# Optimization experiments

Measured on AMD Instinct MI355X. Metric: run time of the kernel, lower is better.

The kernel has to match this reference:

```python
import jax, jax.numpy as jnp
import numpy as np

N = 50000        # nodes
E = 800000       # edges (avg degree 16)
OBS = 128        # observation_dim
HID = 64         # hidden_dim (per head)
H1 = 4           # heads in conv1
ACT = 32         # action_dim
NEG_SLOPE = 0.2  # GATv2 default negative_slope


def setup_inputs() -> dict:
    key = jax.random.key(0)
    ks = jax.random.split(key, 10)
    s = 0.05
    x = jax.random.normal(ks[0], (N, OBS), jnp.float32)
    edge_index = jax.random.randint(ks[1], (2, E), 0, N, dtype=jnp.int32)
    # conv1: GATv2Conv(OBS -> HID, heads=4, concat=True)
    W1l = jax.random.normal(ks[2], (OBS, H1 * HID), jnp.float32) * s  # lin_l (source)
    W1r = jax.random.normal(ks[3], (OBS, H1 * HID), jnp.float32) * s  # lin_r (target)
    att1 = jax.random.normal(ks[4], (H1, HID), jnp.float32) * s
    b1 = jnp.zeros((H1 * HID,), jnp.float32)
    # conv2: GATv2Conv(H1*HID -> ACT, heads=1, concat=False)
    W2l = jax.random.normal(ks[5], (H1 * HID, ACT), jnp.float32) * s
    W2r = jax.random.normal(ks[6], (H1 * HID, ACT), jnp.float32) * s
    att2 = jax.random.normal(ks[7], (1, ACT), jnp.float32) * s
    b2 = jnp.zeros((ACT,), jnp.float32)
    return {"x": x, "edge_index": edge_index, "W1l": W1l, "W1r": W1r,
            "att1": att1, "b1": b1, "W2l": W2l, "W2r": W2r,
            "att2": att2, "b2": b2}


def gatv2_layer(x, Wl, Wr, att, bias, src, dst, heads, out_ch, concat):
    """PyG GATv2Conv (add_self_loops=False, share_weights=False)."""
    n = x.shape[0]
    xl = (x @ Wl).reshape(n, heads, out_ch)  # source transform
    xr = (x @ Wr).reshape(n, heads, out_ch)  # target transform
    e = xl[src] + xr[dst]                    # [E, H, C] gathered messages
    g = jnp.where(e > 0, e, NEG_SLOPE * e)   # LeakyReLU
    logits = jnp.einsum('ehc,hc->eh', g, att)  # [E, H]
    # segment softmax over incoming edges of each destination node
    m = jax.ops.segment_max(logits, dst, num_segments=n)      # [N, H]
    ex = jnp.exp(logits - m[dst])
    denom = jax.ops.segment_sum(ex, dst, num_segments=n)      # [N, H]
    alpha = ex / denom[dst]                                   # [E, H]
    out = jax.ops.segment_sum(xl[src] * alpha[:, :, None], dst, num_segments=n)
    out = out.reshape(n, heads * out_ch) if concat else out.mean(axis=1)
    return out + bias


def reference(x, edge_index, W1l, W1r, att1, b1, W2l, W2r, att2, b2):
    src, dst = edge_index[0], edge_index[1]
    h = jax.nn.relu(gatv2_layer(x, W1l, W1r, att1, b1, src, dst, H1, HID, True))
    out = gatv2_layer(h, W2l, W2r, att2, b2, src, dst, 1, ACT, False)
    return out
```

## Files before the change

kernel.cpp:

```cpp
#include <hip/hip_runtime.h>
#include <hip/hip_bf16.h>
#include <math.h>


#define OBS 128
#define HID 64
#define H1 4
#define C1 256
#define ACT 32
#define PAD 128
#define NEG_SLOPE 0.2f
#define LOG2E 1.4426950408889634f
#define SB 512
#define CAP 8192
#define AGGB 2048

typedef __attribute__((ext_vector_type(2))) _Float16 h2;
typedef __attribute__((ext_vector_type(8))) _Float16 half8;
typedef __attribute__((ext_vector_type(4))) float f32x4;

__device__ inline h2 bc_h2(unsigned u) { return __builtin_bit_cast(h2, u); }
__device__ inline unsigned bc_u(h2 v) { return __builtin_bit_cast(unsigned, v); }
__device__ inline h2 lrelu2(h2 e) {
  const h2 k = {(_Float16)NEG_SLOPE, (_Float16)NEG_SLOPE};
  return __builtin_elementwise_max(e, e * k);
}

__global__ void prep0(const float* __restrict__ W1l, const float* __restrict__ W1r,
                      const float* __restrict__ W2l, const float* __restrict__ W2r,
                      _Float16* __restrict__ W1t, _Float16* __restrict__ W2t,
                      unsigned* __restrict__ bucketCursor) {
  int i = blockIdx.x * 256 + threadIdx.x;
  if (i < 256) bucketCursor[i] = 0;
  if (i < 512 * 128) {
    int n = i >> 7, k = i & 127;
    float v = (n < C1) ? W1l[k * C1 + n] : W1r[k * C1 + (n - C1)];
    W1t[i] = (_Float16)v;
  }
  int j = i - 512 * 128;
  if (j >= 0 && j < 64 * 256) {
    int n = j >> 8, c = j & 255;
    float v = (n < ACT) ? W2l[c * ACT + n] : W2r[c * ACT + (n - ACT)];
    W2t[j] = (_Float16)v;
  }
}

__global__ __launch_bounds__(256) void scat2_k(const int* __restrict__ src,
                                               const int* __restrict__ dst,
                                               unsigned* __restrict__ bucketCursor,
                                               unsigned* __restrict__ sorted,
                                               int E, int epb) {
  __shared__ unsigned cnt[256];
  __shared__ unsigned lbase[256];
  __shared__ unsigned lrank[256];
  int t = threadIdx.x;
  cnt[t] = 0;
  lrank[t] = 0;
  __syncthreads();
  int beg = blockIdx.x * epb;
  int end = beg + epb;
  if (end > E) end = E;
  for (int e = beg + t; e < end; e += 256)
    atomicAdd(&cnt[dst[e] >> 8], 1u);
  __syncthreads();
  unsigned c = cnt[t];
  lbase[t] = c ? atomicAdd(&bucketCursor[t], c) : 0u;
  __syncthreads();
  for (int e = beg + t; e < end; e += 256) {
    int d = dst[e];
    int sv = src[e];
    int b = d >> 8;
    unsigned r = atomicAdd(&lrank[b], 1u);
    sorted[(size_t)b * CAP + lbase[b] + r] =
        ((unsigned)(d & 255) << 16) | (unsigned)sv;
  }
}

__global__ __launch_bounds__(256) void bcsr_k(const unsigned* __restrict__ sorted,
                                              const unsigned* __restrict__ bucketCursor,
                                              unsigned short* __restrict__ esrc_p,
                                              int* __restrict__ cursor, int N) {
  __shared__ unsigned cnt2[256];
  int b = blockIdx.x;
  int t = threadIdx.x;
  cnt2[t] = 0;
  __syncthreads();
  unsigned total = bucketCursor[b];
  const unsigned* sp = sorted + (size_t)b * CAP;
  for (unsigned e = t; e < total; e += 256) {
    unsigned u = sp[e];
    unsigned dl = u >> 16;
    unsigned slot = atomicAdd(&cnt2[dl], 1u);
    if (slot < PAD)
      esrc_p[((size_t)((b << 8) + (int)dl) << 7) + slot] =
          (unsigned short)(u & 0xFFFFu);
  }
  __syncthreads();
  int node = (b << 8) + t;
  if (node < N) cursor[node] = (int)cnt2[t];
}

__global__ __launch_bounds__(256) void gemm1(
    const float* __restrict__ xf,
    const _Float16* __restrict__ W1t,
    _Float16* __restrict__ XLh,
    _Float16* __restrict__ XRh,
    int M) {
  const int LDK = 136;
  __shared__ _Float16 As[128 * 136];
  __shared__ _Float16 Bs[128 * 136];

  const int tid = threadIdx.x;
  const int lane = tid & 63;
  const int wid = tid >> 6;
  const int wm = (wid & 1) * 64, wn = (wid >> 1) * 64;
  const int rowBase = blockIdx.x * 128;
  const int l15 = lane & 15, lq = lane >> 4;

#pragma unroll
  for (int cc = 0; cc < 8; ++cc) {
    int q = cc * 256 + tid;
    int r = q >> 4;
    int kc = (q & 15) * 8;
    int grow = rowBase + r;
    float4 f0 = make_float4(0.f, 0.f, 0.f, 0.f), f1 = f0;
    if (grow < M) {
      f0 = *(const float4*)(xf + (size_t)grow * 128 + kc);
      f1 = *(const float4*)(xf + (size_t)grow * 128 + kc + 4);
    }
    h2 p0 = {(_Float16)f0.x, (_Float16)f0.y};
    h2 p1 = {(_Float16)f0.z, (_Float16)f0.w};
    h2 p2 = {(_Float16)f1.x, (_Float16)f1.y};
    h2 p3 = {(_Float16)f1.z, (_Float16)f1.w};
    *(int4*)(As + r * LDK + kc) = make_int4(bc_u(p0), bc_u(p1), bc_u(p2), bc_u(p3));
  }
#pragma unroll
  for (int cc = 0; cc < 8; ++cc) {
    int q = cc * 256 + tid;
    int r = q >> 4;
    int kc = (q & 15) * 8;
    *(int4*)(Bs + r * LDK + kc) = *(const int4*)(W1t + (size_t)r * 128 + kc);
  }
  __syncthreads();

  for (int cb = 0; cb < 4; ++cb) {
    f32x4 acc[4][4];
#pragma unroll
    for (int i = 0; i < 4; ++i)
#pragma unroll
      for (int j = 0; j < 4; ++j) acc[i][j] = (f32x4){0.f, 0.f, 0.f, 0.f};

#pragma unroll
    for (int ks = 0; ks < 4; ++ks) {
      half8 af[4], bf[4];
#pragma unroll
      for (int t = 0; t < 4; ++t) {
        af[t] = *(const half8*)(As + (wm + t * 16 + l15) * LDK + ks * 32 + lq * 8);
        bf[t] = *(const half8*)(Bs + (wn + t * 16 + l15) * LDK + ks * 32 + lq * 8);
      }
#pragma unroll
      for (int mt = 0; mt < 4; ++mt)
#pragma unroll
        for (int nt = 0; nt < 4; ++nt)
          acc[mt][nt] = __builtin_amdgcn_mfma_f32_16x16x32_f16(
              af[mt], bf[nt], acc[mt][nt], 0, 0, 0);
    }

    _Float16* outp = (cb < 2) ? XLh : XRh;
    int colBase = (cb & 1) * 128;
#pragma unroll
    for (int mt = 0; mt < 4; ++mt) {
#pragma unroll
      for (int r = 0; r < 4; ++r) {
        int row = rowBase + wm + mt * 16 + lq * 4 + r;
        if (row >= M) continue;
#pragma unroll
        for (int nt = 0; nt < 4; ++nt) {
          int col = colBase + wn + nt * 16 + l15;
          outp[(size_t)row * C1 + col] = (_Float16)acc[mt][nt][r];
        }
      }
    }

    if (cb < 3) {
      __syncthreads();
#pragma unroll
      for (int cc = 0; cc < 8; ++cc) {
        int q = cc * 256 + tid;
        int r = q >> 4;
        int kc = (q & 15) * 8;
        *(int4*)(Bs + r * LDK + kc) =
            *(const int4*)(W1t + (size_t)((cb + 1) * 128 + r) * 128 + kc);
      }
      __syncthreads();
    }
  }
}

__global__ __launch_bounds__(256) void gemm_mfma2(
    const _Float16* __restrict__ Hh,
    const _Float16* __restrict__ W2t,
    _Float16* __restrict__ H2h,
    int M) {
  const int LDK = 136;
  __shared__ _Float16 As[128 * 136];
  __shared__ _Float16 Bs[64 * 136];
  const int tid = threadIdx.x;
  const int lane = tid & 63;
  const int wid = tid >> 6;
  const int wm = (wid & 1) * 64, wn = (wid >> 1) * 32;
  const int rowBase = blockIdx.x * 128;

  f32x4 acc[4][2];
#pragma unroll
  for (int i = 0; i < 4; ++i)
#pragma unroll
    for (int j = 0; j < 2; ++j) acc[i][j] = (f32x4){0.f, 0.f, 0.f, 0.f};

  const int l15 = lane & 15, lq = lane >> 4;

  for (int kb = 0; kb < 256; kb += 128) {
#pragma unroll
    for (int cc = 0; cc < 8; ++cc) {
      int q = cc * 256 + tid;
      int r = q >> 4;
      int kc = (q & 15) * 8;
      int grow = rowBase + r;
      int4 av = make_int4(0, 0, 0, 0);
      if (grow < M) av = *(const int4*)(Hh + (size_t)grow * 256 + kb + kc);
      *(int4*)(As + r * LDK + kc) = av;
    }
#pragma unroll
    for (int cc = 0; cc < 4; ++cc) {
      int q = cc * 256 + tid;
      int r = q >> 4;
      int kc = (q & 15) * 8;
      *(int4*)(Bs + r * LDK + kc) = *(const int4*)(W2t + (size_t)r * 256 + kb + kc);
    }
    __syncthreads();

#pragma unroll
    for (int ks = 0; ks < 4; ++ks) {
      half8 af[4], bf[2];
#pragma unroll
      for (int t = 0; t < 4; ++t)
        af[t] = *(const half8*)(As + (wm + t * 16 + l15) * LDK + ks * 32 + lq * 8);
#pragma unroll
      for (int t = 0; t < 2; ++t)
        bf[t] = *(const half8*)(Bs + (wn + t * 16 + l15) * LDK + ks * 32 + lq * 8);
#pragma unroll
      for (int mt = 0; mt < 4; ++mt)
#pragma unroll
        for (int nt = 0; nt < 2; ++nt)
          acc[mt][nt] = __builtin_amdgcn_mfma_f32_16x16x32_f16(
              af[mt], bf[nt], acc[mt][nt], 0, 0, 0);
    }
    __syncthreads();
  }

#pragma unroll
  for (int mt = 0; mt < 4; ++mt) {
#pragma unroll
    for (int r = 0; r < 4; ++r) {
      int row = rowBase + wm + mt * 16 + lq * 4 + r;
      if (row >= M) continue;
#pragma unroll
      for (int nt = 0; nt < 2; ++nt) {
        int col = wn + nt * 16 + l15;
        H2h[(size_t)row * 64 + col] = (_Float16)acc[mt][nt][r];
      }
    }
  }
}

__global__ __launch_bounds__(256) void agg1(const _Float16* __restrict__ XLh,
                                            const _Float16* XRh,
                                            const float* __restrict__ att1,
                                            const float* __restrict__ b1,
                                            const int* __restrict__ degp,
                                            const unsigned short* __restrict__ esrc_p,
                                            _Float16* Hh, int n_nodes) {
  int wave = threadIdx.x >> 6;
  int lane = threadIdx.x & 63;
  int wgid = blockIdx.x * 4 + wave;
  int W = gridDim.x * 4;
  int sl = lane & 31;
  int half = lane >> 5;
  int c8 = sl * 8;

  const char* XLb = (const char*)XLh + c8 * 2;
  const float* ap = att1 + (c8 >> 6) * HID + (c8 & 63);
  float4 a0 = *(const float4*)ap;
  float4 a1 = *(const float4*)(ap + 4);
  h2 av[4] = {{(_Float16)(a0.x * LOG2E), (_Float16)(a0.y * LOG2E)},
              {(_Float16)(a0.z * LOG2E), (_Float16)(a0.w * LOG2E)},
              {(_Float16)(a1.x * LOG2E), (_Float16)(a1.y * LOG2E)},
              {(_Float16)(a1.z * LOG2E), (_Float16)(a1.w * LOG2E)}};
  float4 b0 = *(const float4*)(b1 + c8);
  float4 b3 = *(const float4*)(b1 + c8 + 4);

  for (int n = wgid; n < n_nodes; n += W) {
    int4 xru = *(const int4*)((const char*)XRh + ((size_t)n << 9) + c8 * 2);
    h2 xr[4] = {bc_h2(xru.x), bc_h2(xru.y), bc_h2(xru.z), bc_h2(xru.w)};

    int d = min(degp[n], PAD);
    const unsigned short* ep = esrc_p + ((size_t)n << 7);
    float l = 0.f;
    h2 acc[4];
#pragma unroll
    for (int k = 0; k < 4; ++k) acc[k] = (h2){(_Float16)0.f, (_Float16)0.f};

    int base = 0;
    for (; base + 16 <= d; base += 16) {
      int4 u[8];
#pragma unroll
      for (int t = 0; t < 8; ++t) {
        int s = ep[base + 2 * t + half];
        u[t] = *(const int4*)(XLb + ((size_t)s << 9));
      }
      float c[8];
#pragma unroll
      for (int t = 0; t < 8; ++t) {
        h2 xa = bc_h2(u[t].x), xb = bc_h2(u[t].y), xc = bc_h2(u[t].z), xd = bc_h2(u[t].w);
        float cc = __builtin_amdgcn_fdot2(lrelu2(xa + xr[0]), av[0], 0.f, false);
        cc = __builtin_amdgcn_fdot2(lrelu2(xb + xr[1]), av[1], cc, false);
        cc = __builtin_amdgcn_fdot2(lrelu2(xc + xr[2]), av[2], cc, false);
        cc = __builtin_amdgcn_fdot2(lrelu2(xd + xr[3]), av[3], cc, false);
        c[t] = cc;
      }
#pragma unroll
      for (int t = 0; t < 8; ++t) {
        c[t] += __shfl_xor(c[t], 1);
        c[t] += __shfl_xor(c[t], 2);
        c[t] += __shfl_xor(c[t], 4);
      }
#pragma unroll
      for (int t = 0; t < 8; ++t) {
        float p = __builtin_amdgcn_exp2f(c[t]);
        l += p;
        _Float16 ph = (_Float16)p;
        h2 w = {ph, ph};
        acc[0] = acc[0] + w * bc_h2(u[t].x);
        acc[1] = acc[1] + w * bc_h2(u[t].y);
        acc[2] = acc[2] + w * bc_h2(u[t].z);
        acc[3] = acc[3] + w * bc_h2(u[t].w);
      }
    }
    for (; base + 4 <= d; base += 4) {
      int s0 = ep[base + half];
      int s1 = ep[base + 2 + half];
      int4 u0 = *(const int4*)(XLb + ((size_t)s0 << 9));
      int4 u1 = *(const int4*)(XLb + ((size_t)s1 << 9));
      h2 x0[4] = {bc_h2(u0.x), bc_h2(u0.y), bc_h2(u0.z), bc_h2(u0.w)};
      h2 x1[4] = {bc_h2(u1.x), bc_h2(u1.y), bc_h2(u1.z), bc_h2(u1.w)};
      float c0 = 0.f, c1 = 0.f;
#pragma unroll
      for (int k = 0; k < 4; ++k) {
        c0 = __builtin_amdgcn_fdot2(lrelu2(x0[k] + xr[k]), av[k], c0, false);
        c1 = __builtin_amdgcn_fdot2(lrelu2(x1[k] + xr[k]), av[k], c1, false);
      }
      c0 += __shfl_xor(c0, 1); c1 += __shfl_xor(c1, 1);
      c0 += __shfl_xor(c0, 2); c1 += __shfl_xor(c1, 2);
      c0 += __shfl_xor(c0, 4); c1 += __shfl_xor(c1, 4);
      float p0 = __builtin_amdgcn_exp2f(c0);
      float p1 = __builtin_amdgcn_exp2f(c1);
      l += p0 + p1;
      _Float16 q0 = (_Float16)p0, q1 = (_Float16)p1;
      h2 w0 = {q0, q0}, w1 = {q1, q1};
#pragma unroll
      for (int k = 0; k < 4; ++k) acc[k] = acc[k] + w0 * x0[k] + w1 * x1[k];
    }
    if (base < d) {
      int e0 = base + half, e1 = base + 2 + half;
      bool v0 = e0 < d, v1 = e1 < d;
      int s0 = ep[v0 ? e0 : 0];
      int s1 = ep[v1 ? e1 : 0];
      int4 u0 = *(const int4*)(XLb + ((size_t)s0 << 9));
      int4 u1 = *(const int4*)(XLb + ((size_t)s1 << 9));
      h2 x0[4] = {bc_h2(u0.x), bc_h2(u0.y), bc_h2(u0.z), bc_h2(u0.w)};
      h2 x1[4] = {bc_h2(u1.x), bc_h2(u1.y), bc_h2(u1.z), bc_h2(u1.w)};
      float c0 = 0.f, c1 = 0.f;
#pragma unroll
      for (int k = 0; k < 4; ++k) {
        c0 = __builtin_amdgcn_fdot2(lrelu2(x0[k] + xr[k]), av[k], c0, false);
        c1 = __builtin_amdgcn_fdot2(lrelu2(x1[k] + xr[k]), av[k], c1, false);
      }
      c0 += __shfl_xor(c0, 1); c1 += __shfl_xor(c1, 1);
      c0 += __shfl_xor(c0, 2); c1 += __shfl_xor(c1, 2);
      c0 += __shfl_xor(c0, 4); c1 += __shfl_xor(c1, 4);
      float p0 = v0 ? __builtin_amdgcn_exp2f(c0) : 0.f;
      float p1 = v1 ? __builtin_amdgcn_exp2f(c1) : 0.f;
      l += p0 + p1;
      _Float16 q0 = (_Float16)p0, q1 = (_Float16)p1;
      h2 w0 = {q0, q0}, w1 = {q1, q1};
#pragma unroll
      for (int k = 0; k < 4; ++k) acc[k] = acc[k] + w0 * x0[k] + w1 * x1[k];
    }

    l += __shfl_xor(l, 32);
#pragma unroll
    for (int k = 0; k < 4; ++k) {
      unsigned o = __shfl_xor((int)bc_u(acc[k]), 32);
      acc[k] = acc[k] + bc_h2(o);
    }

    float inv = (d > 0) ? 1.f / l : 0.f;
    if (half == 0) {
      float o0 = fmaxf((float)acc[0][0] * inv + b0.x, 0.f);
      float o1 = fmaxf((float)acc[0][1] * inv + b0.y, 0.f);
      float o2 = fmaxf((float)acc[1][0] * inv + b0.z, 0.f);
      float o3 = fmaxf((float)acc[1][1] * inv + b0.w, 0.f);
      float o4 = fmaxf((float)acc[2][0] * inv + b3.x, 0.f);
      float o5 = fmaxf((float)acc[2][1] * inv + b3.y, 0.f);
      float o6 = fmaxf((float)acc[3][0] * inv + b3.z, 0.f);
      float o7 = fmaxf((float)acc[3][1] * inv + b3.w, 0.f);
      h2 q0 = {(_Float16)o0, (_Float16)o1};
      h2 q1 = {(_Float16)o2, (_Float16)o3};
      h2 q2 = {(_Float16)o4, (_Float16)o5};
      h2 q3 = {(_Float16)o6, (_Float16)o7};
      *(int4*)((char*)Hh + ((size_t)n << 9) + c8 * 2) =
          make_int4(bc_u(q0), bc_u(q1), bc_u(q2), bc_u(q3));
    }
  }
}

__global__ __launch_bounds__(256) void agg2(const _Float16* __restrict__ H2h,
                                            const float* __restrict__ att2,
                                            const float* __restrict__ b2,
                                            const int* __restrict__ degp,
                                            const unsigned short* __restrict__ esrc_p,
                                            float* __restrict__ out, int n_nodes) {
  int wave = threadIdx.x >> 6;
  int lane = threadIdx.x & 63;
  int wgid = blockIdx.x * 4 + wave;
  int W = gridDim.x * 4;
  int g = lane >> 3;
  int j = lane & 7;
  int c4 = j * 4;

  const char* Hb = (const char*)H2h + c4 * 2;
  float4 af = *(const float4*)(att2 + c4);
  h2 a0 = {(_Float16)(af.x * LOG2E), (_Float16)(af.y * LOG2E)};
  h2 a1 = {(_Float16)(af.z * LOG2E), (_Float16)(af.w * LOG2E)};
  float4 bb = *(const float4*)(b2 + c4);

  for (int n = wgid; n < n_nodes; n += W) {
    uint2 hru = *(const uint2*)((const char*)H2h + ((size_t)n << 7) + 64 + c4 * 2);
    h2 hr0 = bc_h2(hru.x), hr1 = bc_h2(hru.y);

    int d = min(degp[n], PAD);
    const unsigned short* ep = esrc_p + ((size_t)n << 7);
    float l = 0.f;
    h2 acc0 = {(_Float16)0.f, (_Float16)0.f}, acc1 = acc0;

    int base = 0;
    for (; base + 16 <= d; base += 16) {
      int s0 = ep[base + g];
      int s1 = ep[base + 8 + g];
      uint2 u0 = *(const uint2*)(Hb + ((size_t)s0 << 7));
      uint2 u1 = *(const uint2*)(Hb + ((size_t)s1 << 7));
      h2 h00 = bc_h2(u0.x), h01 = bc_h2(u0.y);
      h2 h10 = bc_h2(u1.x), h11 = bc_h2(u1.y);
      float c0 = __builtin_amdgcn_fdot2(lrelu2(h00 + hr0), a0,
                 __builtin_amdgcn_fdot2(lrelu2(h01 + hr1), a1, 0.f, false), false);
      float c1 = __builtin_amdgcn_fdot2(lrelu2(h10 + hr0), a0,
                 __builtin_amdgcn_fdot2(lrelu2(h11 + hr1), a1, 0.f, false), false);
      c0 += __shfl_xor(c0, 1); c1 += __shfl_xor(c1, 1);
      c0 += __shfl_xor(c0, 2); c1 += __shfl_xor(c1, 2);
      c0 += __shfl_xor(c0, 4); c1 += __shfl_xor(c1, 4);
      float p0 = __builtin_amdgcn_exp2f(c0);
      float p1 = __builtin_amdgcn_exp2f(c1);
      l += p0 + p1;
      _Float16 q0 = (_Float16)p0, q1 = (_Float16)p1;
      h2 w0 = {q0, q0}, w1 = {q1, q1};
      acc0 = acc0 + w0 * h00 + w1 * h10;
      acc1 = acc1 + w0 * h01 + w1 * h11;
    }
    for (; base + 8 <= d; base += 8) {
      int s = ep[base + g];
      uint2 u = *(const uint2*)(Hb + ((size_t)s << 7));
      h2 h0 = bc_h2(u.x), h1 = bc_h2(u.y);
      float c = __builtin_amdgcn_fdot2(lrelu2(h0 + hr0), a0,
                __builtin_amdgcn_fdot2(lrelu2(h1 + hr1), a1, 0.f, false), false);
      c += __shfl_xor(c, 1);
      c += __shfl_xor(c, 2);
      c += __shfl_xor(c, 4);
      float p = __builtin_amdgcn_exp2f(c);
      l += p;
      _Float16 ph = (_Float16)p;
      h2 p2 = {ph, ph};
      acc0 = acc0 + p2 * h0;
      acc1 = acc1 + p2 * h1;
    }
    if (base < d) {
      int e = base + g;
      bool v = e < d;
      int s = ep[v ? e : 0];
      uint2 u = *(const uint2*)(Hb + ((size_t)s << 7));
      h2 h0 = bc_h2(u.x), h1 = bc_h2(u.y);
      float c = __builtin_amdgcn_fdot2(lrelu2(h0 + hr0), a0,
                __builtin_amdgcn_fdot2(lrelu2(h1 + hr1), a1, 0.f, false), false);
      c += __shfl_xor(c, 1);
      c += __shfl_xor(c, 2);
      c += __shfl_xor(c, 4);
      float p = v ? __builtin_amdgcn_exp2f(c) : 0.f;
      l += p;
      _Float16 ph = (_Float16)p;
      h2 p2 = {ph, ph};
      acc0 = acc0 + p2 * h0;
      acc1 = acc1 + p2 * h1;
    }

#pragma unroll
    for (int o = 8; o < 64; o <<= 1) {
      l += __shfl_xor(l, o);
      acc0 = acc0 + bc_h2((unsigned)__shfl_xor((int)bc_u(acc0), o));
      acc1 = acc1 + bc_h2((unsigned)__shfl_xor((int)bc_u(acc1), o));
    }

    float inv = (d > 0) ? 1.f / l : 0.f;
    if (g == 0) {
      float4 o;
      o.x = (float)acc0[0] * inv + bb.x;
      o.y = (float)acc0[1] * inv + bb.y;
      o.z = (float)acc1[0] * inv + bb.z;
      o.w = (float)acc1[1] * inv + bb.w;
      *(float4*)(out + (size_t)n * ACT + c4) = o;
    }
  }
}

extern "C" void kernel_launch(void* const* d_in, const int* in_sizes, int n_in,
                              void* d_out, int out_size, void* d_ws, size_t ws_size,
                              hipStream_t stream) {
  (void)n_in; (void)out_size; (void)ws_size;
  const float* x    = (const float*)d_in[0];
  const int*   ei   = (const int*)d_in[1];
  const float* W1l  = (const float*)d_in[2];
  const float* W1r  = (const float*)d_in[3];
  const float* att1 = (const float*)d_in[4];
  const float* b1   = (const float*)d_in[5];
  const float* W2l  = (const float*)d_in[6];
  const float* W2r  = (const float*)d_in[7];
  const float* att2 = (const float*)d_in[8];
  const float* b2   = (const float*)d_in[9];
  float* out = (float*)d_out;

  const int N = in_sizes[0] / OBS;
  const int E = in_sizes[1] / 2;
  const int* src = ei;
  const int* dst = ei + E;

  _Float16* XLh = (_Float16*)d_ws;
  _Float16* XRh = XLh + (size_t)N * C1;
  _Float16* W1t = XRh + (size_t)N * C1;
  _Float16* W2t = W1t + 512 * 128;
  int* cursor   = (int*)(W2t + 64 * 256);
  unsigned short* esrc_p = (unsigned short*)(cursor + N);
  _Float16* Hh  = XRh;
  _Float16* H2h = XLh;

  unsigned* sortedW = (unsigned*)d_ws;
  unsigned* bcur    = sortedW + 256 * CAP;

  dim3 b256(256);
  int gemmBlocks = (N + 127) / 128;
  int prepBlocks = (512 * 128 + 64 * 256 + 255) / 256;
  int NB = (N + 255) >> 8;
  int epb = (E + SB - 1) / SB;
  int aggBlocks = AGGB;
  if (aggBlocks * 4 > N) aggBlocks = (N + 3) / 4;

  prep0<<<prepBlocks, b256, 0, stream>>>(W1l, W1r, W2l, W2r, W1t, W2t, bcur);
  scat2_k<<<SB, b256, 0, stream>>>(src, dst, bcur, sortedW, E, epb);
  bcsr_k<<<NB, b256, 0, stream>>>(sortedW, bcur, esrc_p, cursor, N);
  gemm1<<<gemmBlocks, b256, 0, stream>>>(x, W1t, XLh, XRh, N);
  agg1<<<aggBlocks, b256, 0, stream>>>(XLh, XRh, att1, b1, cursor, esrc_p, Hh, N);
  gemm_mfma2<<<gemmBlocks, b256, 0, stream>>>(Hh, W2t, H2h, N);
  agg2<<<aggBlocks, b256, 0, stream>>>(H2h, att2, b2, cursor, esrc_p, out, N);
}
```

Before: 224.5 us.

## Split agg1 into one wave per node-head with eight edges gathered in parallel

The layer-1 aggregation kernel moves from a persistent grid-stride loop, where one wave covers all 256 channels of a node and two edges at a time, to a launch where each wave handles one (node, head) pair. Eight lanes cover the 64 channels of the head and eight edge groups run in parallel, followed by a cross-group shuffle reduction. Blocks are ordered head-major, so concurrently running waves gather only a 128-byte slice of XL per edge, which should improve cache locality and parallelism. The cost is a much larger grid (about 50k blocks), per-head reloads of degree and edge lists, and fewer gathers in flight per lane than the old 16-edge unrolled loop.

After: 249.8 us. +11.3%, slower.

```diff
diff --git a/kernel.cpp b/kernel.cpp
--- a/kernel.cpp
+++ b/kernel.cpp
@@ -279,148 +279,127 @@
                                             const float* __restrict__ b1,
                                             const int* __restrict__ degp,
                                             const unsigned short* __restrict__ esrc_p,
-                                            _Float16* Hh, int n_nodes) {
+                                            _Float16* Hh, int n_nodes, int nb) {
   int wave = threadIdx.x >> 6;
   int lane = threadIdx.x & 63;
-  int wgid = blockIdx.x * 4 + wave;
-  int W = gridDim.x * 4;
-  int sl = lane & 31;
-  int half = lane >> 5;
-  int c8 = sl * 8;
-
-  const char* XLb = (const char*)XLh + c8 * 2;
-  const float* ap = att1 + (c8 >> 6) * HID + (c8 & 63);
+  int head = blockIdx.x / nb;
+  int n = (blockIdx.x - head * nb) * 4 + wave;
+  if (n >= n_nodes) return;
+  int g = lane >> 3;
+  int j = lane & 7;
+  int cb = head * 128 + j * 16;
+
+  const char* XLb = (const char*)XLh + cb;
+  int4 xru = *(const int4*)((const char*)XRh + ((size_t)n << 9) + cb);
+  h2 xr[4] = {bc_h2(xru.x), bc_h2(xru.y), bc_h2(xru.z), bc_h2(xru.w)};
+  const float* ap = att1 + head * HID + j * 8;
   float4 a0 = *(const float4*)ap;
   float4 a1 = *(const float4*)(ap + 4);
   h2 av[4] = {{(_Float16)(a0.x * LOG2E), (_Float16)(a0.y * LOG2E)},
               {(_Float16)(a0.z * LOG2E), (_Float16)(a0.w * LOG2E)},
               {(_Float16)(a1.x * LOG2E), (_Float16)(a1.y * LOG2E)},
               {(_Float16)(a1.z * LOG2E), (_Float16)(a1.w * LOG2E)}};
-  float4 b0 = *(const float4*)(b1 + c8);
-  float4 b3 = *(const float4*)(b1 + c8 + 4);
-
-  for (int n = wgid; n < n_nodes; n += W) {
-    int4 xru = *(const int4*)((const char*)XRh + ((size_t)n << 9) + c8 * 2);
-    h2 xr[4] = {bc_h2(xru.x), bc_h2(xru.y), bc_h2(xru.z), bc_h2(xru.w)};
-
-    int d = min(degp[n], PAD);
-    const unsigned short* ep = esrc_p + ((size_t)n << 7);
-    float l = 0.f;
-    h2 acc[4];
-#pragma unroll
-    for (int k = 0; k < 4; ++k) acc[k] = (h2){(_Float16)0.f, (_Float16)0.f};
-
-    int base = 0;
-    for (; base + 16 <= d; base += 16) {
-      int4 u[8];
-#pragma unroll
-      for (int t = 0; t < 8; ++t) {
-        int s = ep[base + 2 * t + half];
-        u[t] = *(const int4*)(XLb + ((size_t)s << 9));
-      }
-      float c[8];
-#pragma unroll
-      for (int t = 0; t < 8; ++t) {
-        h2 xa = bc_h2(u[t].x), xb = bc_h2(u[t].y), xc = bc_h2(u[t].z), xd = bc_h2(u[t].w);
-        float cc = __builtin_amdgcn_fdot2(lrelu2(xa + xr[0]), av[0], 0.f, false);
-        cc = __builtin_amdgcn_fdot2(lrelu2(xb + xr[1]), av[1], cc, false);
-        cc = __builtin_amdgcn_fdot2(lrelu2(xc + xr[2]), av[2], cc, false);
-        cc = __builtin_amdgcn_fdot2(lrelu2(xd + xr[3]), av[3], cc, false);
-        c[t] = cc;
-      }
-#pragma unroll
-      for (int t = 0; t < 8; ++t) {
-        c[t] += __shfl_xor(c[t], 1);
-        c[t] += __shfl_xor(c[t], 2);
-        c[t] += __shfl_xor(c[t], 4);
-      }
-#pragma unroll
-      for (int t = 0; t < 8; ++t) {
-        float p = __builtin_amdgcn_exp2f(c[t]);
-        l += p;
-        _Float16 ph = (_Float16)p;
-        h2 w = {ph, ph};
-        acc[0] = acc[0] + w * bc_h2(u[t].x);
-        acc[1] = acc[1] + w * bc_h2(u[t].y);
-        acc[2] = acc[2] + w * bc_h2(u[t].z);
-        acc[3] = acc[3] + w * bc_h2(u[t].w);
-      }
-    }
-    for (; base + 4 <= d; base += 4) {
-      int s0 = ep[base + half];
-      int s1 = ep[base + 2 + half];
-      int4 u0 = *(const int4*)(XLb + ((size_t)s0 << 9));
-      int4 u1 = *(const int4*)(XLb + ((size_t)s1 << 9));
-      h2 x0[4] = {bc_h2(u0.x), bc_h2(u0.y), bc_h2(u0.z), bc_h2(u0.w)};
-      h2 x1[4] = {bc_h2(u1.x), bc_h2(u1.y), bc_h2(u1.z), bc_h2(u1.w)};
-      float c0 = 0.f, c1 = 0.f;
-#pragma unroll
-      for (int k = 0; k < 4; ++k) {
-        c0 = __builtin_amdgcn_fdot2(lrelu2(x0[k] + xr[k]), av[k], c0, false);
-        c1 = __builtin_amdgcn_fdot2(lrelu2(x1[k] + xr[k]), av[k], c1, false);
-      }
-      c0 += __shfl_xor(c0, 1); c1 += __shfl_xor(c1, 1);
-      c0 += __shfl_xor(c0, 2); c1 += __shfl_xor(c1, 2);
-      c0 += __shfl_xor(c0, 4); c1 += __shfl_xor(c1, 4);
-      float p0 = __builtin_amdgcn_exp2f(c0);
-      float p1 = __builtin_amdgcn_exp2f(c1);
-      l += p0 + p1;
-      _Float16 q0 = (_Float16)p0, q1 = (_Float16)p1;
-      h2 w0 = {q0, q0}, w1 = {q1, q1};
-#pragma unroll
-      for (int k = 0; k < 4; ++k) acc[k] = acc[k] + w0 * x0[k] + w1 * x1[k];
-    }
-    if (base < d) {
-      int e0 = base + half, e1 = base + 2 + half;
-      bool v0 = e0 < d, v1 = e1 < d;
-      int s0 = ep[v0 ? e0 : 0];
-      int s1 = ep[v1 ? e1 : 0];
-      int4 u0 = *(const int4*)(XLb + ((size_t)s0 << 9));
-      int4 u1 = *(const int4*)(XLb + ((size_t)s1 << 9));
-      h2 x0[4] = {bc_h2(u0.x), bc_h2(u0.y), bc_h2(u0.z), bc_h2(u0.w)};
-      h2 x1[4] = {bc_h2(u1.x), bc_h2(u1.y), bc_h2(u1.z), bc_h2(u1.w)};
-      float c0 = 0.f, c1 = 0.f;
-#pragma unroll
-      for (int k = 0; k < 4; ++k) {
-        c0 = __builtin_amdgcn_fdot2(lrelu2(x0[k] + xr[k]), av[k], c0, false);
-        c1 = __builtin_amdgcn_fdot2(lrelu2(x1[k] + xr[k]), av[k], c1, false);
-      }
-      c0 += __shfl_xor(c0, 1); c1 += __shfl_xor(c1, 1);
-      c0 += __shfl_xor(c0, 2); c1 += __shfl_xor(c1, 2);
-      c0 += __shfl_xor(c0, 4); c1 += __shfl_xor(c1, 4);
-      float p0 = v0 ? __builtin_amdgcn_exp2f(c0) : 0.f;
-      float p1 = v1 ? __builtin_amdgcn_exp2f(c1) : 0.f;
-      l += p0 + p1;
-      _Float16 q0 = (_Float16)p0, q1 = (_Float16)p1;
-      h2 w0 = {q0, q0}, w1 = {q1, q1};
-#pragma unroll
-      for (int k = 0; k < 4; ++k) acc[k] = acc[k] + w0 * x0[k] + w1 * x1[k];
-    }
-
-    l += __shfl_xor(l, 32);
+
+  int d = min(degp[n], PAD);
+  const unsigned short* ep = esrc_p + ((size_t)n << 7);
+  float l = 0.f;
+  h2 acc[4];
+#pragma unroll
+  for (int k = 0; k < 4; ++k) acc[k] = (h2){(_Float16)0.f, (_Float16)0.f};
+
+  int base = 0;
+  for (; base + 16 <= d; base += 16) {
+    int s0 = ep[base + g];
+    int s1 = ep[base + 8 + g];
+    int4 u0 = *(const int4*)(XLb + ((size_t)s0 << 9));
+    int4 u1 = *(const int4*)(XLb + ((size_t)s1 << 9));
+    h2 x0[4] = {bc_h2(u0.x), bc_h2(u0.y), bc_h2(u0.z), bc_h2(u0.w)};
+    h2 x1[4] = {bc_h2(u1.x), bc_h2(u1.y), bc_h2(u1.z), bc_h2(u1.w)};
+    float c0 = 0.f, c1 = 0.f;
 #pragma unroll
     for (int k = 0; k < 4; ++k) {
-      unsigned o = __shfl_xor((int)bc_u(acc[k]), 32);
-      acc[k] = acc[k] + bc_h2(o);
-    }
-
-    float inv = (d > 0) ? 1.f / l : 0.f;
-    if (half == 0) {
-      float o0 = fmaxf((float)acc[0][0] * inv + b0.x, 0.f);
-      float o1 = fmaxf((float)acc[0][1] * inv + b0.y, 0.f);
-      float o2 = fmaxf((float)acc[1][0] * inv + b0.z, 0.f);
-      float o3 = fmaxf((float)acc[1][1] * inv + b0.w, 0.f);
-      float o4 = fmaxf((float)acc[2][0] * inv + b3.x, 0.f);
-      float o5 = fmaxf((float)acc[2][1] * inv + b3.y, 0.f);
-      float o6 = fmaxf((float)acc[3][0] * inv + b3.z, 0.f);
-      float o7 = fmaxf((float)acc[3][1] * inv + b3.w, 0.f);
-      h2 q0 = {(_Float16)o0, (_Float16)o1};
-      h2 q1 = {(_Float16)o2, (_Float16)o3};
-      h2 q2 = {(_Float16)o4, (_Float16)o5};
-      h2 q3 = {(_Float16)o6, (_Float16)o7};
-      *(int4*)((char*)Hh + ((size_t)n << 9) + c8 * 2) =
-          make_int4(bc_u(q0), bc_u(q1), bc_u(q2), bc_u(q3));
-    }
+      c0 = __builtin_amdgcn_fdot2(lrelu2(x0[k] + xr[k]), av[k], c0, false);
+      c1 = __builtin_amdgcn_fdot2(lrelu2(x1[k] + xr[k]), av[k], c1, false);
+    }
+    c0 += __shfl_xor(c0, 1); c1 += __shfl_xor(c1, 1);
+    c0 += __shfl_xor(c0, 2); c1 += __shfl_xor(c1, 2);
+    c0 += __shfl_xor(c0, 4); c1 += __shfl_xor(c1, 4);
+    float p0 = __builtin_amdgcn_exp2f(c0);
+    float p1 = __builtin_amdgcn_exp2f(c1);
+    l += p0 + p1;
+    _Float16 q0 = (_Float16)p0, q1 = (_Float16)p1;
+    h2 w0 = {q0, q0}, w1 = {q1, q1};
+#pragma unroll
+    for (int k = 0; k < 4; ++k) acc[k] = acc[k] + w0 * x0[k] + w1 * x1[k];
+  }
+  for (; base + 8 <= d; base += 8) {
+    int s = ep[base + g];
+    int4 u = *(const int4*)(XLb + ((size_t)s << 9));
+    h2 x0[4] = {bc_h2(u.x), bc_h2(u.y), bc_h2(u.z), bc_h2(u.w)};
+    float c0 = 0.f;
+#pragma unroll
+    for (int k = 0; k < 4; ++k)
+      c0 = __builtin_amdgcn_fdot2(lrelu2(x0[k] + xr[k]), av[k], c0, false);
+    c0 += __shfl_xor(c0, 1);
+    c0 += __shfl_xor(c0, 2);
+    c0 += __shfl_xor(c0, 4);
+    float p0 = __builtin_amdgcn_exp2f(c0);
+    l += p0;
+    _Float16 q0 = (_Float16)p0;
+    h2 w0 = {q0, q0};
+#pragma unroll
+    for (int k = 0; k < 4; ++k) acc[k] = acc[k] + w0 * x0[k];
+  }
+  if (base < d) {
+    int e = base + g;
+    bool v = e < d;
+    int s = ep[v ? e : 0];
+    int4 u = *(const int4*)(XLb + ((size_t)s << 9));
+    h2 x0[4] = {bc_h2(u.x), bc_h2(u.y), bc_h2(u.z), bc_h2(u.w)};
+    float c0 = 0.f;
+#pragma unroll
+    for (int k = 0; k < 4; ++k)
+      c0 = __builtin_amdgcn_fdot2(lrelu2(x0[k] + xr[k]), av[k], c0, false);
+    c0 += __shfl_xor(c0, 1);
+    c0 += __shfl_xor(c0, 2);
+    c0 += __shfl_xor(c0, 4);
+    float p0 = v ? __builtin_amdgcn_exp2f(c0) : 0.f;
+    l += p0;
+    _Float16 q0 = (_Float16)p0;
+    h2 w0 = {q0, q0};
+#pragma unroll
+    for (int k = 0; k < 4; ++k) acc[k] = acc[k] + w0 * x0[k];
+  }
+
+#pragma unroll
+  for (int o = 8; o < 64; o <<= 1) {
+    l += __shfl_xor(l, o);
+#pragma unroll
+    for (int k = 0; k < 4; ++k) {
+      unsigned t = __shfl_xor((int)bc_u(acc[k]), o);
+      acc[k] = acc[k] + bc_h2(t);
+    }
+  }
+
+  float inv = (d > 0) ? 1.f / l : 0.f;
+  if (g == 0) {
+    const float* bp = b1 + head * HID + j * 8;
+    float4 b0 = *(const float4*)bp;
+    float4 b3 = *(const float4*)(bp + 4);
+    float o0 = fmaxf((float)acc[0][0] * inv + b0.x, 0.f);
+    float o1 = fmaxf((float)acc[0][1] * inv + b0.y, 0.f);
+    float o2 = fmaxf((float)acc[1][0] * inv + b0.z, 0.f);
+    float o3 = fmaxf((float)acc[1][1] * inv + b0.w, 0.f);
+    float o4 = fmaxf((float)acc[2][0] * inv + b3.x, 0.f);
+    float o5 = fmaxf((float)acc[2][1] * inv + b3.y, 0.f);
+    float o6 = fmaxf((float)acc[3][0] * inv + b3.z, 0.f);
+    float o7 = fmaxf((float)acc[3][1] * inv + b3.w, 0.f);
+    h2 q0 = {(_Float16)o0, (_Float16)o1};
+    h2 q1 = {(_Float16)o2, (_Float16)o3};
+    h2 q2 = {(_Float16)o4, (_Float16)o5};
+    h2 q3 = {(_Float16)o6, (_Float16)o7};
+    *(int4*)((char*)Hh + ((size_t)n << 9) + cb) =
+        make_int4(bc_u(q0), bc_u(q1), bc_u(q2), bc_u(q3));
   }
 }
 
@@ -568,6 +547,7 @@
   int prepBlocks = (512 * 128 + 64 * 256 + 255) / 256;
   int NB = (N + 255) >> 8;
   int epb = (E + SB - 1) / SB;
+  int nb = (N + 3) / 4;
   int aggBlocks = AGGB;
   if (aggBlocks * 4 > N) aggBlocks = (N + 3) / 4;
 
@@ -575,7 +555,7 @@
   scat2_k<<<SB, b256, 0, stream>>>(src, dst, bcur, sortedW, E, epb);
   bcsr_k<<<NB, b256, 0, stream>>>(sortedW, bcur, esrc_p, cursor, N);
   gemm1<<<gemmBlocks, b256, 0, stream>>>(x, W1t, XLh, XRh, N);
-  agg1<<<aggBlocks, b256, 0, stream>>>(XLh, XRh, att1, b1, cursor, esrc_p, Hh, N);
+  agg1<<<4 * nb, b256, 0, stream>>>(XLh, XRh, att1, b1, cursor, esrc_p, Hh, N, nb);
   gemm_mfma2<<<gemmBlocks, b256, 0, stream>>>(Hh, W2t, H2h, N);
   agg2<<<aggBlocks, b256, 0, stream>>>(H2h, att2, b2, cursor, esrc_p, out, N);
 }
```
